# Kernel optimization log

Hardware: AMD Instinct MI355X
Metric: run time of the kernel (lower is better)

## Reference

```python
import jax, jax.numpy as jnp
import numpy as np

B, LQ, D, NH, NL, NP, DFFN = 16, 900, 256, 8, 4, 4, 2048
HD = D // NH
SHAPES = [(128, 128), (64, 64), (32, 32), (16, 16)]
LIN = sum(h * w for h, w in SHAPES)


def setup_inputs():
    ks = jax.random.split(jax.random.key(0), 24)
    p = lambda k, s: jax.random.normal(k, s, jnp.float32) * 0.02
    z = lambda s: jnp.zeros(s, jnp.float32)
    return {
        "queries": jax.random.normal(ks[0], (B, LQ, D), jnp.float32),
        "features": jax.random.normal(ks[1], (B, LIN, D), jnp.float32),
        "reference_points": jax.random.uniform(ks[2], (B, LQ, NL, 2), jnp.float32),
        "q_pos": jax.random.normal(ks[3], (B, LQ, D), jnp.float32),
        "in_proj_w": p(ks[4], (3 * D, D)), "in_proj_b": z((3 * D,)),
        "out_proj_w": p(ks[5], (D, D)), "out_proj_b": z((D,)),
        "value_proj_w": p(ks[6], (D, D)), "value_proj_b": z((D,)),
        "samp_w": p(ks[7], (NH * NL * NP * 2, D)),
        "samp_b": jax.random.uniform(ks[8], (NH * NL * NP * 2,), jnp.float32, -0.5, 0.5),
        "attw_w": p(ks[9], (NH * NL * NP, D)), "attw_b": z((NH * NL * NP,)),
        "msout_w": p(ks[10], (D, D)), "msout_b": z((D,)),
        "ffn_w1": p(ks[11], (DFFN, D)), "ffn_b1": z((DFFN,)),
        "ffn_w2": p(ks[12], (D, DFFN)), "ffn_b2": z((D,)),
        "ln1_g": jnp.ones((D,), jnp.float32), "ln1_b": z((D,)),
        "ln2_g": jnp.ones((D,), jnp.float32), "ln2_b": z((D,)),
        "ln3_g": jnp.ones((D,), jnp.float32), "ln3_b": z((D,)),
        "kv_spatial_shapes": np.array(SHAPES, np.int32),
        "level_start_index": np.concatenate([[0], np.cumsum([h * w for h, w in SHAPES])[:-1]]).astype(np.int32),
    }


def _ln(x, g, b, eps=1e-5):
    m = x.mean(-1, keepdims=True)
    v = ((x - m) ** 2).mean(-1, keepdims=True)
    return (x - m) * jax.lax.rsqrt(v + eps) * g + b


def _mha(q, k, v, wqkv, bqkv, wo, bo):
    wq, wk, wv = wqkv[:D], wqkv[D:2 * D], wqkv[2 * D:]
    bq, bk, bv = bqkv[:D], bqkv[D:2 * D], bqkv[2 * D:]
    qh = (q @ wq.T + bq).reshape(B, LQ, NH, HD)
    kh = (k @ wk.T + bk).reshape(B, LQ, NH, HD)
    vh = (v @ wv.T + bv).reshape(B, LQ, NH, HD)
    s = jnp.einsum("bqhd,bkhd->bhqk", qh, kh) / jnp.sqrt(jnp.float32(HD))
    a = jax.nn.softmax(s, axis=-1)
    o = jnp.einsum("bhqk,bkhd->bqhd", a, vh).reshape(B, LQ, D)
    return o @ wo.T + bo


def _ms_deform(value, loc, attw):
    # value (B,LIN,NH,HD); loc (B,LQ,NH,NL,NP,2) normalized; attw (B,LQ,NH,NL,NP)
    out = jnp.zeros((B, LQ, NH, HD), jnp.float32)
    start = 0
    for l, (hl, wl) in enumerate(SHAPES):
        v = value[:, start:start + hl * wl].transpose(0, 2, 1, 3)  # (B,NH,hl*wl,HD)
        g = loc[:, :, :, l]  # (B,LQ,NH,NP,2)
        # grid_sample align_corners=False pixel coords
        x = g[..., 0] * wl - 0.5
        y = g[..., 1] * hl - 0.5
        x0 = jnp.floor(x); y0 = jnp.floor(y)
        fx = x - x0; fy = y - y0
        x0 = x0.astype(jnp.int32); y0 = y0.astype(jnp.int32)
        acc = jnp.zeros((B, LQ, NH, NP, HD), jnp.float32)
        for dy, wy in ((0, 1.0 - fy), (1, fy)):
            for dx, wx in ((0, 1.0 - fx), (1, fx)):
                xi = x0 + dx; yi = y0 + dy
                valid = (xi >= 0) & (xi < wl) & (yi >= 0) & (yi < hl)
                idx = jnp.clip(yi, 0, hl - 1) * wl + jnp.clip(xi, 0, wl - 1)
                idx = idx.transpose(0, 2, 1, 3).reshape(B, NH, LQ * NP)
                s = jnp.take_along_axis(v, idx[..., None], axis=2)
                s = s.reshape(B, NH, LQ, NP, HD).transpose(0, 2, 1, 3, 4)
                w = jnp.where(valid, wy * wx, 0.0)  # zero-padding outside
                acc = acc + s * w[..., None]
        out = out + (acc * attw[:, :, :, l, :, None]).sum(3)
        start += hl * wl
    return out.reshape(B, LQ, D)


def reference(queries, features, reference_points, q_pos, in_proj_w, in_proj_b, out_proj_w, out_proj_b, value_proj_w, value_proj_b, samp_w, samp_b, attw_w, attw_b, msout_w, msout_b, ffn_w1, ffn_b1, ffn_w2, ffn_b2, ln1_g, ln1_b, ln2_g, ln2_b, ln3_g, ln3_b, kv_spatial_shapes, level_start_index):
    qk = queries + q_pos
    x = _ln(queries + _mha(qk, qk, queries, in_proj_w, in_proj_b, out_proj_w, out_proj_b), ln1_g, ln1_b)
    # deformable multi-scale cross attention
    q2 = x + q_pos
    value = (features @ value_proj_w.T + value_proj_b).reshape(B, LIN, NH, HD)
    off = (q2 @ samp_w.T + samp_b).reshape(B, LQ, NH, NL, NP, 2)
    attw = jax.nn.softmax((q2 @ attw_w.T + attw_b).reshape(B, LQ, NH, NL * NP), axis=-1).reshape(B, LQ, NH, NL, NP)
    norm = jnp.stack([jnp.asarray(kv_spatial_shapes)[:, 1], jnp.asarray(kv_spatial_shapes)[:, 0]], -1).astype(jnp.float32)  # (NL,2)=(W,H)
    loc = reference_points[:, :, None, :, None, :] + off / norm[None, None, None, :, None, :]
    ms = _ms_deform(value, loc, attw) @ msout_w.T + msout_b
    x = _ln(x + ms, ln2_g, ln2_b)
    ffn = jax.nn.relu(x @ ffn_w1.T + ffn_b1) @ ffn_w2.T + ffn_b2
    return _ln(x + ffn, ln3_g, ln3_b)
```

## Files before the change

kernel.cpp:

```cpp
#include <hip/hip_runtime.h>
#include <hip/hip_bf16.h>
#include <math.h>

#define B_    16
#define LQ_   900
#define D_    256
#define NH_   8
#define HD_   32
#define NL_   4
#define NP_   4
#define DFFN_ 2048
#define LIN_  21760

typedef unsigned short u16;
typedef __attribute__((ext_vector_type(8))) short bf16x8;
typedef __attribute__((ext_vector_type(4))) float f32x4;

__device__ __forceinline__ short f2bf(float f) {
    unsigned u = __float_as_uint(f);
    u += 0x7fffu + ((u >> 16) & 1u);
    return (short)(u >> 16);
}
__device__ __forceinline__ float bf2f(u16 u) {
    return __uint_as_float(((unsigned)u) << 16);
}

#define WOFF_INPROJ  0
#define WOFF_OUTPROJ 196608
#define WOFF_VALPROJ 262144
#define WOFF_SAMP    327680
#define WOFF_ATTW    393216
#define WOFF_MSOUT   425984
#define WOFF_FFN1    491520
#define WOFF_FFN2    1015808
#define WTOTAL       1540096

__global__ __launch_bounds__(256) void wprep_kernel(const float* __restrict__ s0,
                                                    const float* __restrict__ s1,
                                                    const float* __restrict__ s2,
                                                    const float* __restrict__ s3,
                                                    const float* __restrict__ s4,
                                                    const float* __restrict__ s5,
                                                    const float* __restrict__ s6,
                                                    const float* __restrict__ s7,
                                                    u16* __restrict__ Wb) {
    int i8 = (blockIdx.x * 256 + threadIdx.x) * 8;
    if (i8 >= WTOTAL) return;
    const float* src; int rel;
    if      (i8 < WOFF_OUTPROJ) { src = s0; rel = i8; }
    else if (i8 < WOFF_VALPROJ) { src = s1; rel = i8 - WOFF_OUTPROJ; }
    else if (i8 < WOFF_SAMP)    { src = s2; rel = i8 - WOFF_VALPROJ; }
    else if (i8 < WOFF_ATTW)    { src = s3; rel = i8 - WOFF_SAMP; }
    else if (i8 < WOFF_MSOUT)   { src = s4; rel = i8 - WOFF_ATTW; }
    else if (i8 < WOFF_FFN1)    { src = s5; rel = i8 - WOFF_MSOUT; }
    else if (i8 < WOFF_FFN2)    { src = s6; rel = i8 - WOFF_FFN1; }
    else                        { src = s7; rel = i8 - WOFF_FFN2; }
    float4 v0 = *(const float4*)(src + rel);
    float4 v1 = *(const float4*)(src + rel + 4);
    short o[8];
    o[0] = f2bf(v0.x); o[1] = f2bf(v0.y); o[2] = f2bf(v0.z); o[3] = f2bf(v0.w);
    o[4] = f2bf(v1.x); o[5] = f2bf(v1.y); o[6] = f2bf(v1.z); o[7] = f2bf(v1.w);
    *(bf16x8*)(Wb + i8) = *(bf16x8*)o;
}

__global__ __launch_bounds__(256) void add_bf16_kernel(const float* __restrict__ a,
                                                       const float* __restrict__ b,
                                                       u16* __restrict__ osum,
                                                       u16* __restrict__ oa,
                                                       size_t n4) {
    size_t i = (size_t)blockIdx.x * blockDim.x + threadIdx.x;
    if (i >= n4) return;
    float4 x = ((const float4*)a)[i];
    float4 y = ((const float4*)b)[i];
    ushort4 s;
    s.x = (u16)f2bf(x.x + y.x); s.y = (u16)f2bf(x.y + y.y);
    s.z = (u16)f2bf(x.z + y.z); s.w = (u16)f2bf(x.w + y.w);
    ((ushort4*)osum)[i] = s;
    if (oa) {
        ushort4 q;
        q.x = (u16)f2bf(x.x); q.y = (u16)f2bf(x.y);
        q.z = (u16)f2bf(x.z); q.w = (u16)f2bf(x.w);
        ((ushort4*)oa)[i] = q;
    }
}

#define LDK 40
template <typename TA, typename TC>
__global__ __launch_bounds__(256) void gemm2_kernel(const TA* __restrict__ A,
                                                    const u16* __restrict__ W,
                                                    const float* __restrict__ bias,
                                                    const float* __restrict__ res,
                                                    TC* __restrict__ C,
                                                    int M, int N, int K, int relu) {
    __shared__ __align__(16) u16 As[2][128 * LDK];
    __shared__ __align__(16) u16 Bs[2][128 * LDK];

    const int n0 = blockIdx.x * 128;
    const int m0 = blockIdx.y * 128;
    const int t  = threadIdx.x;

    const int srow = t >> 1;
    const int scol = (t & 1) << 4;

    const int lane = t & 63;
    const int lr   = lane & 15;
    const int kg   = lane >> 4;
    const int wid  = t >> 6;
    const int wr   = wid >> 1;
    const int wc   = wid & 1;

    f32x4 acc[4][4] = {};

    const int  nk  = K >> 5;
    const int  gm  = m0 + srow;
    const bool mok = (gm < M);

    const float* af32 = (const float*)A + (size_t)(mok ? gm : 0) * K + scol;
    const u16*   ab16 = (const u16*)A + (size_t)(mok ? gm : 0) * K + scol;
    const u16*   wp   = W + (size_t)(n0 + srow) * K + scol;

    float4 af[4];
    bf16x8 ab[2];
    bf16x8 wf[2];

    if constexpr (sizeof(TA) == 4) {
        if (mok) {
            #pragma unroll
            for (int q = 0; q < 4; ++q) af[q] = *(const float4*)(af32 + q * 4);
        } else {
            #pragma unroll
            for (int q = 0; q < 4; ++q) af[q] = make_float4(0.f, 0.f, 0.f, 0.f);
        }
    } else {
        if (mok) { ab[0] = *(const bf16x8*)ab16; ab[1] = *(const bf16x8*)(ab16 + 8); }
        else {
            #pragma unroll
            for (int q = 0; q < 8; ++q) { ab[0][q] = 0; ab[1][q] = 0; }
        }
    }
    wf[0] = *(const bf16x8*)wp;
    wf[1] = *(const bf16x8*)(wp + 8);

    for (int kt = 0; kt < nk; ++kt) {
        const int cur = kt & 1;
        if constexpr (sizeof(TA) == 4) {
            short tmp[16];
            #pragma unroll
            for (int q = 0; q < 4; ++q) {
                tmp[q * 4 + 0] = f2bf(af[q].x);
                tmp[q * 4 + 1] = f2bf(af[q].y);
                tmp[q * 4 + 2] = f2bf(af[q].z);
                tmp[q * 4 + 3] = f2bf(af[q].w);
            }
            *(bf16x8*)&As[cur][srow * LDK + scol]     = *(bf16x8*)tmp;
            *(bf16x8*)&As[cur][srow * LDK + scol + 8] = *(bf16x8*)(tmp + 8);
        } else {
            *(bf16x8*)&As[cur][srow * LDK + scol]     = ab[0];
            *(bf16x8*)&As[cur][srow * LDK + scol + 8] = ab[1];
        }
        *(bf16x8*)&Bs[cur][srow * LDK + scol]     = wf[0];
        *(bf16x8*)&Bs[cur][srow * LDK + scol + 8] = wf[1];

        if (kt + 1 < nk) {
            const int k1 = (kt + 1) << 5;
            if constexpr (sizeof(TA) == 4) {
                if (mok) {
                    #pragma unroll
                    for (int q = 0; q < 4; ++q) af[q] = *(const float4*)(af32 + k1 + q * 4);
                }
            } else {
                if (mok) {
                    ab[0] = *(const bf16x8*)(ab16 + k1);
                    ab[1] = *(const bf16x8*)(ab16 + k1 + 8);
                }
            }
            wf[0] = *(const bf16x8*)(wp + k1);
            wf[1] = *(const bf16x8*)(wp + k1 + 8);
        }

        __syncthreads();

        const u16* pA = &As[cur][(wr * 64 + lr) * LDK + kg * 8];
        const u16* pB = &Bs[cur][(wc * 64 + lr) * LDK + kg * 8];
        bf16x8 a[4], b[4];
        #pragma unroll
        for (int i = 0; i < 4; ++i) a[i] = *(const bf16x8*)(pA + i * 16 * LDK);
        #pragma unroll
        for (int j = 0; j < 4; ++j) b[j] = *(const bf16x8*)(pB + j * 16 * LDK);
        #pragma unroll
        for (int i = 0; i < 4; ++i)
            #pragma unroll
            for (int j = 0; j < 4; ++j)
                acc[i][j] = __builtin_amdgcn_mfma_f32_16x16x32_bf16(a[i], b[j], acc[i][j], 0, 0, 0);
    }

    #pragma unroll
    for (int i = 0; i < 4; ++i) {
        #pragma unroll
        for (int j = 0; j < 4; ++j) {
            const int n = n0 + wc * 64 + j * 16 + lr;
            const float bn = bias[n];
            #pragma unroll
            for (int r = 0; r < 4; ++r) {
                const int m = m0 + wr * 64 + i * 16 + kg * 4 + r;
                if (m < M) {
                    float v = acc[i][j][r] + bn;
                    if (res)  v += res[(size_t)m * N + n];
                    if (relu) v = fmaxf(v, 0.f);
                    if constexpr (sizeof(TC) == 4) C[(size_t)m * N + n] = v;
                    else                           C[(size_t)m * N + n] = (TC)(u16)f2bf(v);
                }
            }
        }
    }
}

#define LDA2 40
#define LDP  72
__global__ __launch_bounds__(256) void attn_mfma_kernel(const u16* __restrict__ Qg,
                                                        const u16* __restrict__ Kg,
                                                        const u16* __restrict__ Vg,
                                                        u16* __restrict__ Og) {
    __shared__ __align__(16) u16 Ks[64 * LDA2];
    __shared__ __align__(16) u16 Vs[64 * LDA2];
    __shared__ __align__(16) u16 Ps[4][16 * LDP];

    const int qt = blockIdx.x, h = blockIdx.y, b = blockIdx.z;
    const int t  = threadIdx.x;
    const int wq = t >> 6;
    const int lane = t & 63;
    const int l15  = lane & 15;
    const int g    = lane >> 4;
    const int q0   = qt * 64;

    const int srow = t >> 2;
    const int sd   = (t & 3) * 8;

    int qrow = q0 + wq * 16 + l15;
    if (qrow > LQ_ - 1) qrow = LQ_ - 1;
    const bf16x8 qfrag = *(const bf16x8*)(Qg + ((size_t)(b * LQ_) + qrow) * D_ + h * HD_ + g * 8);

    float m_i = -1e30f, l_i = 0.f;
    f32x4 o_acc[2] = {};
    const float scale = 0.17677669529663687f;

    for (int k0 = 0; k0 < 960; k0 += 64) {
        {
            int kr = k0 + srow;
            bf16x8 kv, vv;
            if (kr < LQ_) {
                kv = *(const bf16x8*)(Kg + ((size_t)(b * LQ_) + kr) * D_ + h * HD_ + sd);
                vv = *(const bf16x8*)(Vg + ((size_t)(b * LQ_) + kr) * D_ + h * HD_ + sd);
            } else {
                #pragma unroll
                for (int j = 0; j < 8; ++j) { kv[j] = 0; vv[j] = 0; }
            }
            *(bf16x8*)&Ks[srow * LDA2 + sd] = kv;
            *(bf16x8*)&Vs[srow * LDA2 + sd] = vv;
        }
        __syncthreads();

        float p[4][4];
        float tmax = -1e30f;
        #pragma unroll
        for (int kt = 0; kt < 4; ++kt) {
            bf16x8 af = *(const bf16x8*)&Ks[(kt * 16 + l15) * LDA2 + g * 8];
            f32x4 c = {0.f, 0.f, 0.f, 0.f};
            c = __builtin_amdgcn_mfma_f32_16x16x32_bf16(af, qfrag, c, 0, 0, 0);
            #pragma unroll
            for (int r = 0; r < 4; ++r) {
                int kglob = k0 + kt * 16 + g * 4 + r;
                float s = (kglob < LQ_) ? c[r] * scale : -1e30f;
                p[kt][r] = s;
                tmax = fmaxf(tmax, s);
            }
        }
        tmax = fmaxf(tmax, __shfl_xor(tmax, 16));
        tmax = fmaxf(tmax, __shfl_xor(tmax, 32));
        float newm = fmaxf(m_i, tmax);
        float corr = __expf(m_i - newm);
        float rs = 0.f;
        #pragma unroll
        for (int kt = 0; kt < 4; ++kt) {
            #pragma unroll
            for (int r = 0; r < 4; ++r) {
                float e = __expf(p[kt][r] - newm);
                p[kt][r] = e;
                rs += e;
            }
            ushort4 pk;
            pk.x = (u16)f2bf(p[kt][0]);
            pk.y = (u16)f2bf(p[kt][1]);
            pk.z = (u16)f2bf(p[kt][2]);
            pk.w = (u16)f2bf(p[kt][3]);
            *(ushort4*)&Ps[wq][l15 * LDP + kt * 16 + g * 4] = pk;
        }
        rs += __shfl_xor(rs, 16);
        rs += __shfl_xor(rs, 32);
        l_i = l_i * corr + rs;
        m_i = newm;

        #pragma unroll
        for (int r = 0; r < 4; ++r) {
            float cq = __shfl(corr, g * 4 + r);
// ... 14 lines not shown
            }
        }
        __syncthreads();
    }

    float il = 1.f / l_i;
    #pragma unroll
    for (int r = 0; r < 4; ++r) {
        float ilq = __shfl(il, g * 4 + r);
        int q = q0 + wq * 16 + g * 4 + r;
        if (q < LQ_) {
            u16* dst = Og + ((size_t)(b * LQ_) + q) * D_ + h * HD_ + l15;
            dst[0]  = (u16)f2bf(o_acc[0][r] * ilq);
            dst[16] = (u16)f2bf(o_acc[1][r] * ilq);
        }
    }
}

__global__ __launch_bounds__(256) void ln_kernel(const float* __restrict__ X,
                                                 const float* __restrict__ g,
                                                 const float* __restrict__ bb,
                                                 float* __restrict__ Y,
                                                 u16* __restrict__ Yb, int M) {
    int row  = blockIdx.x * 4 + (threadIdx.x >> 6);
    int lane = threadIdx.x & 63;
    if (row >= M) return;
    const float* x = X + (size_t)row * D_;
    float4 v = *(const float4*)(x + lane * 4);
    float s = v.x + v.y + v.z + v.w;
    #pragma unroll
    for (int o = 32; o >= 1; o >>= 1) s += __shfl_xor(s, o);
    float mean = s * (1.f / D_);
    float dx0 = v.x - mean, dx1 = v.y - mean, dx2 = v.z - mean, dx3 = v.w - mean;
    float ss = dx0 * dx0 + dx1 * dx1 + dx2 * dx2 + dx3 * dx3;
    #pragma unroll
    for (int o = 32; o >= 1; o >>= 1) ss += __shfl_xor(ss, o);
    float rstd = rsqrtf(ss * (1.f / D_) + 1e-5f);
    float4 gv = *(const float4*)(g + lane * 4);
    float4 bv = *(const float4*)(bb + lane * 4);
    float4 out;
    out.x = dx0 * rstd * gv.x + bv.x;
    out.y = dx1 * rstd * gv.y + bv.y;
    out.z = dx2 * rstd * gv.z + bv.z;
    out.w = dx3 * rstd * gv.w + bv.w;
    *(float4*)(Y + (size_t)row * D_ + lane * 4) = out;
    if (Yb) {
        ushort4 ob;
        ob.x = (u16)f2bf(out.x); ob.y = (u16)f2bf(out.y);
        ob.z = (u16)f2bf(out.z); ob.w = (u16)f2bf(out.w);
        *(ushort4*)(Yb + (size_t)row * D_ + lane * 4) = ob;
    }
}

__global__ __launch_bounds__(256) void softmax16_kernel(const float* __restrict__ X,
                                                        float* __restrict__ Y,
                                                        int rows) {
    int r = blockIdx.x * blockDim.x + threadIdx.x;
    if (r >= rows) return;
    const float* x = X + (size_t)r * 16;
    float m = -1e30f;
    #pragma unroll
    for (int i = 0; i < 16; ++i) m = fmaxf(m, x[i]);
    float e[16], s = 0.f;
    #pragma unroll
    for (int i = 0; i < 16; ++i) { e[i] = expf(x[i] - m); s += e[i]; }
    float inv = 1.f / s;
    float* y = Y + (size_t)r * 16;
    #pragma unroll
    for (int i = 0; i < 16; ++i) y[i] = e[i] * inv;
}

__global__ __launch_bounds__(256) void msdeform2_kernel(const u16* __restrict__ value,
                                                        const float* __restrict__ ref,
                                                        const float* __restrict__ off,
                                                        const float* __restrict__ attw,
                                                        u16* __restrict__ out) {
    const int levH[4] = {128, 64, 32, 16};
    const int levW[4] = {128, 64, 32, 16};
    const int levS[4] = {0, 16384, 20480, 21504};

    int gid = blockIdx.x * 256 + threadIdx.x;
    int d8  = gid & 3;
    int bqh = gid >> 2;
    int h   = bqh & (NH_ - 1);
    int bq  = bqh >> 3;
    int b   = bq / LQ_;

    const float* refp = ref  + (size_t)bq * NL_ * 2;
    const float* offp = off  + (size_t)bq * 256 + h * 32;
    const float* awp  = attw + (size_t)bq * 128 + h * 16;
    const u16* vbase  = value + (size_t)b * LIN_ * D_ + h * HD_ + d8 * 8;

    float acc[8] = {};
    #pragma unroll
    for (int l = 0; l < NL_; ++l) {
        float rx = refp[l * 2 + 0], ry = refp[l * 2 + 1];
        const int wl = levW[l], hl = levH[l];
        const u16* vlev = vbase + (size_t)levS[l] * D_;
        #pragma unroll
        for (int p = 0; p < NP_; ++p) {
            float ox = offp[(l * NP_ + p) * 2 + 0];
            float oy = offp[(l * NP_ + p) * 2 + 1];
            float x = rx * wl + ox - 0.5f;
            float y = ry * hl + oy - 0.5f;
            float x0f = floorf(x), y0f = floorf(y);
            float fx = x - x0f, fy = y - y0f;
            int x0 = (int)x0f, y0 = (int)y0f;
            float aw = awp[l * NP_ + p];
            #pragma unroll
            for (int dy = 0; dy < 2; ++dy) {
                int   yi = y0 + dy;
                float wy = dy ? fy : 1.f - fy;
                bool  vy = (yi >= 0) && (yi < hl);
                int   yc = min(max(yi, 0), hl - 1);
                #pragma unroll
                for (int dx = 0; dx < 2; ++dx) {
                    int   xi = x0 + dx;
                    float wx = dx ? fx : 1.f - fx;
                    bool  vx = (xi >= 0) && (xi < wl);
                    int   xc = min(max(xi, 0), wl - 1);
                    float w  = (vx && vy) ? aw * wy * wx : 0.f;
                    bf16x8 v = *(const bf16x8*)(vlev + (size_t)(yc * wl + xc) * D_);
                    #pragma unroll
                    for (int j = 0; j < 8; ++j)
                        acc[j] += w * bf2f((u16)v[j]);
                }
            }
        }
    }
    short o[8];
    #pragma unroll
    for (int j = 0; j < 8; ++j) o[j] = f2bf(acc[j]);
    *(bf16x8*)(out + (size_t)bq * D_ + h * HD_ + d8 * 8) = *(bf16x8*)o;
}

extern "C" void kernel_launch(void* const* d_in, const int* in_sizes, int n_in,
                              void* d_out, int out_size, void* d_ws, size_t ws_size,
                              hipStream_t stream) {
    const float* queries      = (const float*)d_in[0];
    const float* features     = (const float*)d_in[1];
    const float* refpts       = (const float*)d_in[2];
    const float* q_pos        = (const float*)d_in[3];
    const float* in_proj_w    = (const float*)d_in[4];
    const float* in_proj_b    = (const float*)d_in[5];
    const float* out_proj_w   = (const float*)d_in[6];
    const float* out_proj_b   = (const float*)d_in[7];
    const float* value_proj_w = (const float*)d_in[8];
    const float* value_proj_b = (const float*)d_in[9];
    const float* samp_w       = (const float*)d_in[10];
    const float* samp_b       = (const float*)d_in[11];
    const float* attw_w       = (const float*)d_in[12];
    const float* attw_b       = (const float*)d_in[13];
    const float* msout_w      = (const float*)d_in[14];
    const float* msout_b      = (const float*)d_in[15];
    const float* ffn_w1       = (const float*)d_in[16];
    const float* ffn_b1       = (const float*)d_in[17];
    const float* ffn_w2       = (const float*)d_in[18];
    const float* ffn_b2       = (const float*)d_in[19];
    const float* ln1_g        = (const float*)d_in[20];
    const float* ln1_b        = (const float*)d_in[21];
    const float* ln2_g        = (const float*)d_in[22];
    const float* ln2_b        = (const float*)d_in[23];
    const float* ln3_g        = (const float*)d_in[24];
    const float* ln3_b        = (const float*)d_in[25];

    float* ws = (float*)d_ws;
    const size_t NQ = (size_t)B_ * LQ_ * D_;
    float* bufB = ws;
    float* bufC = ws + NQ;
    float* bufF = ws + 2 * NQ;
    float* bufD = ws + 3 * NQ;
    u16* U    = (u16*)(ws + 4 * NQ);
    u16* qkb  = U;
    u16* qb   = U + NQ;
    u16* q2b  = U + 2 * NQ;
    u16* Qb   = U + 3 * NQ;
    u16* Kb   = U + 4 * NQ;
    u16* Vb   = U + 5 * NQ;
    u16* Ob   = U + 6 * NQ;
    u16* MSb  = U + 7 * NQ;
    u16* LN2b = U + 8 * NQ;
    u16* VALb = U + 9 * NQ;
    u16* H1b  = VALb + (size_t)B_ * LIN_ * D_;
    u16* Wb   = H1b + (size_t)B_ * LQ_ * DFFN_;

    const int M  = B_ * LQ_;
    const int MV = B_ * LIN_;
    const int GY = (M + 127) / 128;

    wprep_kernel<<<752, 256, 0, stream>>>(in_proj_w, out_proj_w, value_proj_w, samp_w,
                                          attw_w, msout_w, ffn_w1, ffn_w2, Wb);

    add_bf16_kernel<<<3600, 256, 0, stream>>>(queries, q_pos, qkb, qb, NQ / 4);

    gemm2_kernel<u16, u16><<<dim3(2, GY), 256, 0, stream>>>(qkb, Wb + WOFF_INPROJ,          in_proj_b,       nullptr, Qb, M, 256, 256, 0);
    gemm2_kernel<u16, u16><<<dim3(2, GY), 256, 0, stream>>>(qkb, Wb + WOFF_INPROJ + 65536,  in_proj_b + 256, nullptr, Kb, M, 256, 256, 0);
    gemm2_kernel<u16, u16><<<dim3(2, GY), 256, 0, stream>>>(qb,  Wb + WOFF_INPROJ + 131072, in_proj_b + 512, nullptr, Vb, M, 256, 256, 0);

    attn_mfma_kernel<<<dim3(15, NH_, B_), 256, 0, stream>>>(Qb, Kb, Vb, Ob);

    gemm2_kernel<u16, float><<<dim3(2, GY), 256, 0, stream>>>(Ob, Wb + WOFF_OUTPROJ, out_proj_b, queries, bufB, M, 256, 256, 0);
    ln_kernel<<<3600, 256, 0, stream>>>(bufB, ln1_g, ln1_b, bufF, nullptr, M);

    add_bf16_kernel<<<3600, 256, 0, stream>>>(bufF, q_pos, q2b, nullptr, NQ / 4);

    gemm2_kernel<float, u16><<<dim3(2, MV / 128), 256, 0, stream>>>(features, Wb + WOFF_VALPROJ, value_proj_b, nullptr, VALb, MV, 256, 256, 0);

    gemm2_kernel<u16, float><<<dim3(2, GY), 256, 0, stream>>>(q2b, Wb + WOFF_SAMP, samp_b, nullptr, bufB, M, 256, 256, 0);
    gemm2_kernel<u16, float><<<dim3(1, GY), 256, 0, stream>>>(q2b, Wb + WOFF_ATTW, attw_b, nullptr, bufC, M, 128, 256, 0);

    softmax16_kernel<<<450, 256, 0, stream>>>(bufC, bufD, B_ * LQ_ * NH_);

    msdeform2_kernel<<<1800, 256, 0, stream>>>(VALb, refpts, bufB, bufD, MSb);

    gemm2_kernel<u16, float><<<dim3(2, GY), 256, 0, stream>>>(MSb, Wb + WOFF_MSOUT, msout_b, bufF, bufB, M, 256, 256, 0);
    ln_kernel<<<3600, 256, 0, stream>>>(bufB, ln2_g, ln2_b, bufC, LN2b, M);

    gemm2_kernel<u16, u16><<<dim3(16, GY), 256, 0, stream>>>(LN2b, Wb + WOFF_FFN1, ffn_b1, nullptr, H1b, M, 2048, 256, 1);

    gemm2_kernel<u16, float><<<dim3(2, GY), 256, 0, stream>>>(H1b, Wb + WOFF_FFN2, ffn_b2, bufC, bufB, M, 256, 2048, 0);
    ln_kernel<<<3600, 256, 0, stream>>>(bufB, ln3_g, ln3_b, (float*)d_out, nullptr, M);
}
```

Measured before the change: 1.055 ms.

## Add weight-stationary register GEMM for K=256 layers and fuse Q/K and samp/attw projections

Introduces a wavefront-level weight-stationary GEMM that keeps a 32-column slice of the weight in registers and streams 16-row A tiles with double-buffered loads, skipping LDS and block barriers. It replaces the LDS-tiled GEMM for every K=256 projection. The Q and K projections are merged into one N=512 output, and the sampling-offset and attention-weight projections into one N=384 output, with the attention, softmax and deformable-sampling kernels reindexed to match. A packed bias buffer is prepared, and the workspace is resized for the wider fused output. The trade-off is higher register pressure and more A reloads across column slices in exchange for fewer launches and no LDS staging.

```diff
diff --git a/kernel.cpp b/kernel.cpp
--- a/kernel.cpp
+++ b/kernel.cpp
@@ -63,6 +63,38 @@
     *(bf16x8*)(Wb + i8) = *(bf16x8*)o;
 }
 
+#define BOFF_INPROJ  0
+#define BOFF_OUTPROJ 768
+#define BOFF_VALPROJ 1024
+#define BOFF_SAMPATT 1280
+#define BOFF_MSOUT   1664
+#define BOFF_FFN1    1920
+#define BOFF_FFN2    3968
+#define BTOTAL       4224
+
+__global__ __launch_bounds__(256) void bprep_kernel(const float* __restrict__ b0,
+                                                    const float* __restrict__ b1,
+                                                    const float* __restrict__ b2,
+                                                    const float* __restrict__ b3,
+                                                    const float* __restrict__ b4,
+                                                    const float* __restrict__ b5,
+                                                    const float* __restrict__ b6,
+                                                    const float* __restrict__ b7,
+                                                    float* __restrict__ Bb) {
+    int i = blockIdx.x * 256 + threadIdx.x;
+    if (i >= BTOTAL) return;
+    const float* s; int rel;
+    if      (i < BOFF_OUTPROJ) { s = b0; rel = i; }
+    else if (i < BOFF_VALPROJ) { s = b1; rel = i - BOFF_OUTPROJ; }
+    else if (i < BOFF_SAMPATT) { s = b2; rel = i - BOFF_VALPROJ; }
+    else if (i < 1536)         { s = b3; rel = i - BOFF_SAMPATT; }
+    else if (i < BOFF_MSOUT)   { s = b4; rel = i - 1536; }
+    else if (i < BOFF_FFN1)    { s = b5; rel = i - BOFF_MSOUT; }
+    else if (i < BOFF_FFN2)    { s = b6; rel = i - BOFF_FFN1; }
+    else                       { s = b7; rel = i - BOFF_FFN2; }
+    Bb[i] = s[rel];
+}
+
 __global__ __launch_bounds__(256) void add_bf16_kernel(const float* __restrict__ a,
                                                        const float* __restrict__ b,
                                                        u16* __restrict__ osum,
@@ -84,6 +116,113 @@
     }
 }
 
+template <typename TA, typename TC>
+__global__ __launch_bounds__(256) void wsgemm_kernel(const TA* __restrict__ A,
+                                                     const u16* __restrict__ W,
+                                                     const float* __restrict__ bias,
+                                                     const float* __restrict__ res,
+                                                     TC* __restrict__ C,
+                                                     int MT, int NS, int CH, int N, int relu) {
+    const int lane = threadIdx.x & 63;
+    const int l15  = lane & 15;
+    const int g    = lane >> 4;
+    const int wid  = blockIdx.x * 4 + (threadIdx.x >> 6);
+    const int nchunks = (MT + CH - 1) / CH;
+    if (wid >= NS * nchunks) return;
+    const int ns = wid % NS;
+    const int n0 = ns * 32;
+    int mt = (wid / NS) * CH;
+    const int mtend = (mt + CH < MT) ? mt + CH : MT;
+
+    bf16x8 w0[8], w1[8];
+    {
+        const u16* wp0 = W + (size_t)(n0 + l15) * 256 + g * 8;
+        const u16* wp1 = W + (size_t)(n0 + 16 + l15) * 256 + g * 8;
+        #pragma unroll
+        for (int ks = 0; ks < 8; ++ks) {
+            w0[ks] = *(const bf16x8*)(wp0 + ks * 32);
+            w1[ks] = *(const bf16x8*)(wp1 + ks * 32);
+        }
+    }
+    const float bn0 = bias[n0 + l15];
+    const float bn1 = bias[n0 + 16 + l15];
+
+    auto compute_store = [&](const bf16x8 (&a)[8], int m0) {
+        f32x4 acc0 = {0.f, 0.f, 0.f, 0.f}, acc1 = {0.f, 0.f, 0.f, 0.f};
+        #pragma unroll
+        for (int ks = 0; ks < 8; ++ks) {
+            acc0 = __builtin_amdgcn_mfma_f32_16x16x32_bf16(a[ks], w0[ks], acc0, 0, 0, 0);
+            acc1 = __builtin_amdgcn_mfma_f32_16x16x32_bf16(a[ks], w1[ks], acc1, 0, 0, 0);
+        }
+        #pragma unroll
+        for (int r = 0; r < 4; ++r) {
+            const int m = m0 + g * 4 + r;
+            float v0 = acc0[r] + bn0;
+            float v1 = acc1[r] + bn1;
+            if (res) {
+                v0 += res[(size_t)m * N + n0 + l15];
+                v1 += res[(size_t)m * N + n0 + 16 + l15];
+            }
+            if (relu) { v0 = fmaxf(v0, 0.f); v1 = fmaxf(v1, 0.f); }
+            if constexpr (sizeof(TC) == 4) {
+                C[(size_t)m * N + n0 + l15]      = v0;
+                C[(size_t)m * N + n0 + 16 + l15] = v1;
+            } else {
+                C[(size_t)m * N + n0 + l15]      = (TC)(u16)f2bf(v0);
+                C[(size_t)m * N + n0 + 16 + l15] = (TC)(u16)f2bf(v1);
+            }
+        }
+    };
+
+    if constexpr (sizeof(TA) == 2) {
+        const u16* Ab = (const u16*)A;
+        bf16x8 p[8], q[8];
+        {
+            const u16* ar = Ab + (size_t)(mt * 16 + l15) * 256 + g * 8;
+            #pragma unroll
+            for (int ks = 0; ks < 8; ++ks) p[ks] = *(const bf16x8*)(ar + ks * 32);
+        }
+        while (true) {
+            if (mt + 1 < mtend) {
+                const u16* ar = Ab + (size_t)((mt + 1) * 16 + l15) * 256 + g * 8;
+                #pragma unroll
+                for (int ks = 0; ks < 8; ++ks) q[ks] = *(const bf16x8*)(ar + ks * 32);
+            }
+            compute_store(p, mt * 16);
+            if (++mt >= mtend) break;
+            if (mt + 1 < mtend) {
+                const u16* ar = Ab + (size_t)((mt + 1) * 16 + l15) * 256 + g * 8;
+                #pragma unroll
+                for (int ks = 0; ks < 8; ++ks) p[ks] = *(const bf16x8*)(ar + ks * 32);
+            }
+            compute_store(q, mt * 16);
+            if (++mt >= mtend) break;
+        }
+    } else {
+        const float* Af = (const float*)A;
+        for (; mt < mtend; ++mt) {
+            const float* ar = Af + (size_t)(mt * 16 + l15) * 256 + g * 8;
+            float4 f0[8], f1[8];
+            #pragma unroll
+            for (int ks = 0; ks < 8; ++ks) {
+                f0[ks] = *(const float4*)(ar + ks * 32);
+                f1[ks] = *(const float4*)(ar + ks * 32 + 4);
+            }
+            bf16x8 a[8];
+            #pragma unroll
+            for (int ks = 0; ks < 8; ++ks) {
+                short tmp[8];
+                tmp[0] = f2bf(f0[ks].x); tmp[1] = f2bf(f0[ks].y);
+                tmp[2] = f2bf(f0[ks].z); tmp[3] = f2bf(f0[ks].w);
+                tmp[4] = f2bf(f1[ks].x); tmp[5] = f2bf(f1[ks].y);
+                tmp[6] = f2bf(f1[ks].z); tmp[7] = f2bf(f1[ks].w);
+                a[ks] = *(bf16x8*)tmp;
+            }
+            compute_store(a, mt * 16);
+        }
+    }
+}
+
 #define LDK 40
 template <typename TA, typename TC>
 __global__ __launch_bounds__(256) void gemm2_kernel(const TA* __restrict__ A,
@@ -115,64 +254,30 @@
     const int  gm  = m0 + srow;
     const bool mok = (gm < M);
 
-    const float* af32 = (const float*)A + (size_t)(mok ? gm : 0) * K + scol;
-    const u16*   ab16 = (const u16*)A + (size_t)(mok ? gm : 0) * K + scol;
-    const u16*   wp   = W + (size_t)(n0 + srow) * K + scol;
-
-    float4 af[4];
-    bf16x8 ab[2];
-    bf16x8 wf[2];
-
-    if constexpr (sizeof(TA) == 4) {
-        if (mok) {
-            #pragma unroll
-            for (int q = 0; q < 4; ++q) af[q] = *(const float4*)(af32 + q * 4);
-        } else {
-            #pragma unroll
-            for (int q = 0; q < 4; ++q) af[q] = make_float4(0.f, 0.f, 0.f, 0.f);
-        }
-    } else {
-        if (mok) { ab[0] = *(const bf16x8*)ab16; ab[1] = *(const bf16x8*)(ab16 + 8); }
-        else {
-            #pragma unroll
-            for (int q = 0; q < 8; ++q) { ab[0][q] = 0; ab[1][q] = 0; }
-        }
+    const u16* ab16 = (const u16*)A + (size_t)(mok ? gm : 0) * K + scol;
+    const u16* wp   = W + (size_t)(n0 + srow) * K + scol;
+
+    bf16x8 ab[2], wf[2];
+    if (mok) { ab[0] = *(const bf16x8*)ab16; ab[1] = *(const bf16x8*)(ab16 + 8); }
+    else {
+        #pragma unroll
+        for (int q = 0; q < 8; ++q) { ab[0][q] = 0; ab[1][q] = 0; }
     }
     wf[0] = *(const bf16x8*)wp;
     wf[1] = *(const bf16x8*)(wp + 8);
 
     for (int kt = 0; kt < nk; ++kt) {
         const int cur = kt & 1;
-        if constexpr (sizeof(TA) == 4) {
-            short tmp[16];
-            #pragma unroll
-            for (int q = 0; q < 4; ++q) {
-                tmp[q * 4 + 0] = f2bf(af[q].x);
-                tmp[q * 4 + 1] = f2bf(af[q].y);
-                tmp[q * 4 + 2] = f2bf(af[q].z);
-                tmp[q * 4 + 3] = f2bf(af[q].w);
-            }
-            *(bf16x8*)&As[cur][srow * LDK + scol]     = *(bf16x8*)tmp;
-            *(bf16x8*)&As[cur][srow * LDK + scol + 8] = *(bf16x8*)(tmp + 8);
-        } else {
-            *(bf16x8*)&As[cur][srow * LDK + scol]     = ab[0];
-            *(bf16x8*)&As[cur][srow * LDK + scol + 8] = ab[1];
-        }
+        *(bf16x8*)&As[cur][srow * LDK + scol]     = ab[0];
+        *(bf16x8*)&As[cur][srow * LDK + scol + 8] = ab[1];
         *(bf16x8*)&Bs[cur][srow * LDK + scol]     = wf[0];
         *(bf16x8*)&Bs[cur][srow * LDK + scol + 8] = wf[1];
 
         if (kt + 1 < nk) {
             const int k1 = (kt + 1) << 5;
-            if constexpr (sizeof(TA) == 4) {
-                if (mok) {
-                    #pragma unroll
-                    for (int q = 0; q < 4; ++q) af[q] = *(const float4*)(af32 + k1 + q * 4);
-                }
-            } else {
-                if (mok) {
-                    ab[0] = *(const bf16x8*)(ab16 + k1);
-                    ab[1] = *(const bf16x8*)(ab16 + k1 + 8);
-                }
+            if (mok) {
+                ab[0] = *(const bf16x8*)(ab16 + k1);
+                ab[1] = *(const bf16x8*)(ab16 + k1 + 8);
             }
             wf[0] = *(const bf16x8*)(wp + k1);
             wf[1] = *(const bf16x8*)(wp + k1 + 8);
@@ -217,8 +322,7 @@
 
 #define LDA2 40
 #define LDP  72
-__global__ __launch_bounds__(256) void attn_mfma_kernel(const u16* __restrict__ Qg,
-                                                        const u16* __restrict__ Kg,
+__global__ __launch_bounds__(256) void attn_mfma_kernel(const u16* __restrict__ QKg,
                                                         const u16* __restrict__ Vg,
                                                         u16* __restrict__ Og) {
     __shared__ __align__(16) u16 Ks[64 * LDA2];
@@ -238,7 +342,7 @@
 
     int qrow = q0 + wq * 16 + l15;
     if (qrow > LQ_ - 1) qrow = LQ_ - 1;
-    const bf16x8 qfrag = *(const bf16x8*)(Qg + ((size_t)(b * LQ_) + qrow) * D_ + h * HD_ + g * 8);
+    const bf16x8 qfrag = *(const bf16x8*)(QKg + ((size_t)(b * LQ_) + qrow) * 512 + h * HD_ + g * 8);
 
     float m_i = -1e30f, l_i = 0.f;
     f32x4 o_acc[2] = {};
@@ -249,7 +353,7 @@
             int kr = k0 + srow;
             bf16x8 kv, vv;
             if (kr < LQ_) {
-                kv = *(const bf16x8*)(Kg + ((size_t)(b * LQ_) + kr) * D_ + h * HD_ + sd);
+                kv = *(const bf16x8*)(QKg + ((size_t)(b * LQ_) + kr) * 512 + 256 + h * HD_ + sd);
                 vv = *(const bf16x8*)(Vg + ((size_t)(b * LQ_) + kr) * D_ + h * HD_ + sd);
             } else {
                 #pragma unroll
@@ -370,12 +474,12 @@
     }
 }
 
-__global__ __launch_bounds__(256) void softmax16_kernel(const float* __restrict__ X,
-                                                        float* __restrict__ Y,
-                                                        int rows) {
+__global__ __launch_bounds__(256) void softmax16v_kernel(const float* __restrict__ X,
+                                                         float* __restrict__ Y,
+                                                         int rows) {
     int r = blockIdx.x * blockDim.x + threadIdx.x;
     if (r >= rows) return;
-    const float* x = X + (size_t)r * 16;
+    const float* x = X + (size_t)(r >> 3) * 384 + 256 + (r & 7) * 16;
     float m = -1e30f;
     #pragma unroll
     for (int i = 0; i < 16; ++i) m = fmaxf(m, x[i]);
@@ -405,7 +509,7 @@
     int b   = bq / LQ_;
 
     const float* refp = ref  + (size_t)bq * NL_ * 2;
-    const float* offp = off  + (size_t)bq * 256 + h * 32;
+    const float* offp = off  + (size_t)bq * 384 + h * 32;
     const float* awp  = attw + (size_t)bq * 128 + h * 16;
     const u16* vbase  = value + (size_t)b * LIN_ * D_ + h * HD_ + d8 * 8;
 
@@ -485,15 +589,14 @@
     float* ws = (float*)d_ws;
     const size_t NQ = (size_t)B_ * LQ_ * D_;
     float* bufB = ws;
-    float* bufC = ws + NQ;
-    float* bufF = ws + 2 * NQ;
-    float* bufD = ws + 3 * NQ;
-    u16* U    = (u16*)(ws + 4 * NQ);
+    float* bufC = ws + 3 * NQ / 2;
+    float* bufF = bufC + NQ;
+    float* bufD = bufF + NQ;
+    u16* U    = (u16*)(bufD + NQ);
     u16* qkb  = U;
     u16* qb   = U + NQ;
     u16* q2b  = U + 2 * NQ;
-    u16* Qb   = U + 3 * NQ;
-    u16* Kb   = U + 4 * NQ;
+    u16* QKb  = U + 3 * NQ;
     u16* Vb   = U + 5 * NQ;
     u16* Ob   = U + 6 * NQ;
     u16* MSb  = U + 7 * NQ;
@@ -501,41 +604,40 @@
     u16* VALb = U + 9 * NQ;
     u16* H1b  = VALb + (size_t)B_ * LIN_ * D_;
     u16* Wb   = H1b + (size_t)B_ * LQ_ * DFFN_;
-
-    const int M  = B_ * LQ_;
-    const int MV = B_ * LIN_;
-    const int GY = (M + 127) / 128;
+    float* Bb = (float*)(Wb + WTOTAL);
+
+    const int M = B_ * LQ_;
 
     wprep_kernel<<<752, 256, 0, stream>>>(in_proj_w, out_proj_w, value_proj_w, samp_w,
                                           attw_w, msout_w, ffn_w1, ffn_w2, Wb);
+    bprep_kernel<<<17, 256, 0, stream>>>(in_proj_b, out_proj_b, value_proj_b, samp_b,
+                                         attw_b, msout_b, ffn_b1, ffn_b2, Bb);
 
     add_bf16_kernel<<<3600, 256, 0, stream>>>(queries, q_pos, qkb, qb, NQ / 4);
 
-    gemm2_kernel<u16, u16><<<dim3(2, GY), 256, 0, stream>>>(qkb, Wb + WOFF_INPROJ,          in_proj_b,       nullptr, Qb, M, 256, 256, 0);
-    gemm2_kernel<u16, u16><<<dim3(2, GY), 256, 0, stream>>>(qkb, Wb + WOFF_INPROJ + 65536,  in_proj_b + 256, nullptr, Kb, M, 256, 256, 0);
-    gemm2_kernel<u16, u16><<<dim3(2, GY), 256, 0, stream>>>(qb,  Wb + WOFF_INPROJ + 131072, in_proj_b + 512, nullptr, Vb, M, 256, 256, 0);
-
-    attn_mfma_kernel<<<dim3(15, NH_, B_), 256, 0, stream>>>(Qb, Kb, Vb, Ob);
-
-    gemm2_kernel<u16, float><<<dim3(2, GY), 256, 0, stream>>>(Ob, Wb + WOFF_OUTPROJ, out_proj_b, queries, bufB, M, 256, 256, 0);
-    ln_kernel<<<3600, 256, 0, stream>>>(bufB, ln1_g, ln1_b, bufF, nullptr, M);
+    wsgemm_kernel<u16, u16><<<900, 256, 0, stream>>>(qkb, Wb + WOFF_INPROJ, Bb + BOFF_INPROJ, nullptr, QKb, 900, 16, 4, 512, 0);
+    wsgemm_kernel<u16, u16><<<450, 256, 0, stream>>>(qb, Wb + WOFF_INPROJ + 131072, Bb + BOFF_INPROJ + 512, nullptr, Vb, 900, 8, 4, 256, 0);
+
+    attn_mfma_kernel<<<dim3(15, NH_, B_), 256, 0, stream>>>(QKb, Vb, Ob);
+
+    wsgemm_kernel<u16, float><<<450, 256, 0, stream>>>(Ob, Wb + WOFF_OUTPROJ, Bb + BOFF_OUTPROJ, queries, bufC, 900, 8, 4, 256, 0);
+    ln_kernel<<<3600, 256, 0, stream>>>(bufC, ln1_g, ln1_b, bufF, nullptr, M);
 
     add_bf16_kernel<<<3600, 256, 0, stream>>>(bufF, q_pos, q2b, nullptr, NQ / 4);
 
-    gemm2_kernel<float, u16><<<dim3(2, MV / 128), 256, 0, stream>>>(features, Wb + WOFF_VALPROJ, value_proj_b, nullptr, VALb, MV, 256, 256, 0);
-
-    gemm2_kernel<u16, float><<<dim3(2, GY), 256, 0, stream>>>(q2b, Wb + WOFF_SAMP, samp_b, nullptr, bufB, M, 256, 256, 0);
-    gemm2_kernel<u16, float><<<dim3(1, GY), 256, 0, stream>>>(q2b, Wb + WOFF_ATTW, attw_b, nullptr, bufC, M, 128, 256, 0);
-
-    softmax16_kernel<<<450, 256, 0, stream>>>(bufC, bufD, B_ * LQ_ * NH_);
+    wsgemm_kernel<float, u16><<<1360, 256, 0, stream>>>(features, Wb + WOFF_VALPROJ, Bb + BOFF_VALPROJ, nullptr, VALb, 21760, 8, 32, 256, 0);
+
+    wsgemm_kernel<u16, float><<<675, 256, 0, stream>>>(q2b, Wb + WOFF_SAMP, Bb + BOFF_SAMPATT, nullptr, bufB, 900, 12, 4, 384, 0);
+
+    softmax16v_kernel<<<450, 256, 0, stream>>>(bufB, bufD, B_ * LQ_ * NH_);
 
     msdeform2_kernel<<<1800, 256, 0, stream>>>(VALb, refpts, bufB, bufD, MSb);
 
-    gemm2_kernel<u16, float><<<dim3(2, GY), 256, 0, stream>>>(MSb, Wb + WOFF_MSOUT, msout_b, bufF, bufB, M, 256, 256, 0);
-    ln_kernel<<<3600, 256, 0, stream>>>(bufB, ln2_g, ln2_b, bufC, LN2b, M);
-
-    gemm2_kernel<u16, u16><<<dim3(16, GY), 256, 0, stream>>>(LN2b, Wb + WOFF_FFN1, ffn_b1, nullptr, H1b, M, 2048, 256, 1);
-
-    gemm2_kernel<u16, float><<<dim3(2, GY), 256, 0, stream>>>(H1b, Wb + WOFF_FFN2, ffn_b2, bufC, bufB, M, 256, 2048, 0);
-    ln_kernel<<<3600, 256, 0, stream>>>(bufB, ln3_g, ln3_b, (float*)d_out, nullptr, M);
-}
+    wsgemm_kernel<u16, float><<<450, 256, 0, stream>>>(MSb, Wb + WOFF_MSOUT, Bb + BOFF_MSOUT, bufF, bufC, 900, 8, 4, 256, 0);
+    ln_kernel<<<3600, 256, 0, stream>>>(bufC, ln2_g, ln2_b, bufD, LN2b, M);
+
+    wsgemm_kernel<u16, u16><<<3600, 256, 0, stream>>>(LN2b, Wb + WOFF_FFN1, Bb + BOFF_FFN1, nullptr, H1b, 900, 64, 4, 2048, 1);
+
+    gemm2_kernel<u16, float><<<dim3(2, 113), 256, 0, stream>>>(H1b, Wb + WOFF_FFN2, ffn_b2, bufD, bufC, M, 256, 2048, 0);
+    ln_kernel<<<3600, 256, 0, stream>>>(bufC, ln3_g, ln3_b, (float*)d_out, nullptr, M);
+}
```

After: 1.402 ms. 32.9% more time.

## Merge Q/K and sampling/attention projections, deepen GEMM global prefetch

Applied to the files above, without the earlier changes.

Q and K projections become a single N=512 GEMM writing an interleaved QK buffer, which the attention kernel now reads with stride 512. The sampling-offset and attention-weight projections become a single N=384 GEMM, and the softmax and deformable kernels index into that combined layout. The GEMM kernel now keeps two register stages of global loads in flight ahead of the LDS write. Biases are packed into a contiguous buffer so the concatenated projections see contiguous biases. The intent is fewer launches, one fewer read of the shared input, and better hiding of global-load latency, at the cost of more registers in the GEMM.

```diff
diff --git a/kernel.cpp b/kernel.cpp
--- a/kernel.cpp
+++ b/kernel.cpp
@@ -63,6 +63,38 @@
     *(bf16x8*)(Wb + i8) = *(bf16x8*)o;
 }
 
+#define BOFF_INPROJ  0
+#define BOFF_OUTPROJ 768
+#define BOFF_VALPROJ 1024
+#define BOFF_SAMPATT 1280
+#define BOFF_MSOUT   1664
+#define BOFF_FFN1    1920
+#define BOFF_FFN2    3968
+#define BTOTAL       4224
+
+__global__ __launch_bounds__(256) void bprep_kernel(const float* __restrict__ b0,
+                                                    const float* __restrict__ b1,
+                                                    const float* __restrict__ b2,
+                                                    const float* __restrict__ b3,
+                                                    const float* __restrict__ b4,
+                                                    const float* __restrict__ b5,
+                                                    const float* __restrict__ b6,
+                                                    const float* __restrict__ b7,
+                                                    float* __restrict__ Bb) {
+    int i = blockIdx.x * 256 + threadIdx.x;
+    if (i >= BTOTAL) return;
+    const float* s; int rel;
+    if      (i < BOFF_OUTPROJ) { s = b0; rel = i; }
+    else if (i < BOFF_VALPROJ) { s = b1; rel = i - BOFF_OUTPROJ; }
+    else if (i < BOFF_SAMPATT) { s = b2; rel = i - BOFF_VALPROJ; }
+    else if (i < 1536)         { s = b3; rel = i - BOFF_SAMPATT; }
+    else if (i < BOFF_MSOUT)   { s = b4; rel = i - 1536; }
+    else if (i < BOFF_FFN1)    { s = b5; rel = i - BOFF_MSOUT; }
+    else if (i < BOFF_FFN2)    { s = b6; rel = i - BOFF_FFN1; }
+    else                       { s = b7; rel = i - BOFF_FFN2; }
+    Bb[i] = s[rel];
+}
+
 __global__ __launch_bounds__(256) void add_bf16_kernel(const float* __restrict__ a,
                                                        const float* __restrict__ b,
                                                        u16* __restrict__ osum,
@@ -86,7 +118,7 @@
 
 #define LDK 40
 template <typename TA, typename TC>
-__global__ __launch_bounds__(256) void gemm2_kernel(const TA* __restrict__ A,
+__global__ __launch_bounds__(256) void gemm3_kernel(const TA* __restrict__ A,
                                                     const u16* __restrict__ W,
                                                     const float* __restrict__ bias,
                                                     const float* __restrict__ res,
@@ -98,10 +130,8 @@
     const int n0 = blockIdx.x * 128;
     const int m0 = blockIdx.y * 128;
     const int t  = threadIdx.x;
-
     const int srow = t >> 1;
     const int scol = (t & 1) << 4;
-
     const int lane = t & 63;
     const int lr   = lane & 15;
     const int kg   = lane >> 4;
@@ -119,69 +149,42 @@
     const u16*   ab16 = (const u16*)A + (size_t)(mok ? gm : 0) * K + scol;
     const u16*   wp   = W + (size_t)(n0 + srow) * K + scol;
 
-    float4 af[4];
-    bf16x8 ab[2];
-    bf16x8 wf[2];
-
-    if constexpr (sizeof(TA) == 4) {
-        if (mok) {
-            #pragma unroll
-            for (int q = 0; q < 4; ++q) af[q] = *(const float4*)(af32 + q * 4);
-        } else {
-            #pragma unroll
-            for (int q = 0; q < 4; ++q) af[q] = make_float4(0.f, 0.f, 0.f, 0.f);
-        }
-    } else {
-        if (mok) { ab[0] = *(const bf16x8*)ab16; ab[1] = *(const bf16x8*)(ab16 + 8); }
-        else {
-            #pragma unroll
-            for (int q = 0; q < 8; ++q) { ab[0][q] = 0; ab[1][q] = 0; }
-        }
-    }
-    wf[0] = *(const bf16x8*)wp;
-    wf[1] = *(const bf16x8*)(wp + 8);
-
-    for (int kt = 0; kt < nk; ++kt) {
-        const int cur = kt & 1;
-        if constexpr (sizeof(TA) == 4) {
-            short tmp[16];
-            #pragma unroll
-            for (int q = 0; q < 4; ++q) {
-                tmp[q * 4 + 0] = f2bf(af[q].x);
-                tmp[q * 4 + 1] = f2bf(af[q].y);
-                tmp[q * 4 + 2] = f2bf(af[q].z);
-                tmp[q * 4 + 3] = f2bf(af[q].w);
-            }
-            *(bf16x8*)&As[cur][srow * LDK + scol]     = *(bf16x8*)tmp;
-            *(bf16x8*)&As[cur][srow * LDK + scol + 8] = *(bf16x8*)(tmp + 8);
-        } else {
-            *(bf16x8*)&As[cur][srow * LDK + scol]     = ab[0];
-            *(bf16x8*)&As[cur][srow * LDK + scol + 8] = ab[1];
-        }
-        *(bf16x8*)&Bs[cur][srow * LDK + scol]     = wf[0];
-        *(bf16x8*)&Bs[cur][srow * LDK + scol + 8] = wf[1];
-
-        if (kt + 1 < nk) {
-            const int k1 = (kt + 1) << 5;
-            if constexpr (sizeof(TA) == 4) {
-                if (mok) {
-                    #pragma unroll
-                    for (int q = 0; q < 4; ++q) af[q] = *(const float4*)(af32 + k1 + q * 4);
-                }
-            } else {
-                if (mok) {
-                    ab[0] = *(const bf16x8*)(ab16 + k1);
-                    ab[1] = *(const bf16x8*)(ab16 + k1 + 8);
-                }
-            }
-            wf[0] = *(const bf16x8*)(wp + k1);
-            wf[1] = *(const bf16x8*)(wp + k1 + 8);
-        }
-
-        __syncthreads();
-
-        const u16* pA = &As[cur][(wr * 64 + lr) * LDK + kg * 8];
-        const u16* pB = &Bs[cur][(wc * 64 + lr) * LDK + kg * 8];
+    float4 af0[4], af1[4];
+    bf16x8 ab0[2], ab1[2];
+    bf16x8 wf0[2], wf1[2];
+    if (!mok) {
+        #pragma unroll
+        for (int q = 0; q < 4; ++q) af0[q] = af1[q] = make_float4(0.f, 0.f, 0.f, 0.f);
+        #pragma unroll
+        for (int q = 0; q < 8; ++q) { ab0[0][q] = 0; ab0[1][q] = 0; ab1[0][q] = 0; ab1[1][q] = 0; }
+    }
+
+#define GLOAD_A_F(afX, kt_) do { if (mok) { \
+        _Pragma("unroll") for (int q = 0; q < 4; ++q) afX[q] = *(const float4*)(af32 + ((kt_) << 5) + q * 4); } } while (0)
+#define GLOAD_A_B(abX, kt_) do { if (mok) { \
+        abX[0] = *(const bf16x8*)(ab16 + ((kt_) << 5)); \
+        abX[1] = *(const bf16x8*)(ab16 + ((kt_) << 5) + 8); } } while (0)
+#define GLOAD_W(wfX, kt_) do { \
+        wfX[0] = *(const bf16x8*)(wp + ((kt_) << 5)); \
+        wfX[1] = *(const bf16x8*)(wp + ((kt_) << 5) + 8); } while (0)
+
+#define DSWRITE(bufI, afX, abX, wfX) do { \
+        if constexpr (sizeof(TA) == 4) { \
+            short tmp[16]; \
+            _Pragma("unroll") for (int q = 0; q < 4; ++q) { \
+                tmp[q * 4 + 0] = f2bf(afX[q].x); tmp[q * 4 + 1] = f2bf(afX[q].y); \
+                tmp[q * 4 + 2] = f2bf(afX[q].z); tmp[q * 4 + 3] = f2bf(afX[q].w); } \
+            *(bf16x8*)&As[bufI][srow * LDK + scol]     = *(bf16x8*)tmp; \
+            *(bf16x8*)&As[bufI][srow * LDK + scol + 8] = *(bf16x8*)(tmp + 8); \
+        } else { \
+            *(bf16x8*)&As[bufI][srow * LDK + scol]     = abX[0]; \
+            *(bf16x8*)&As[bufI][srow * LDK + scol + 8] = abX[1]; } \
+        *(bf16x8*)&Bs[bufI][srow * LDK + scol]     = wfX[0]; \
+        *(bf16x8*)&Bs[bufI][srow * LDK + scol + 8] = wfX[1]; } while (0)
+
+    auto domfma = [&](const u16* bufA, const u16* bufB) {
+        const u16* pA = bufA + (wr * 64 + lr) * LDK + kg * 8;
+        const u16* pB = bufB + (wc * 64 + lr) * LDK + kg * 8;
         bf16x8 a[4], b[4];
         #pragma unroll
         for (int i = 0; i < 4; ++i) a[i] = *(const bf16x8*)(pA + i * 16 * LDK);
@@ -192,7 +195,35 @@
             #pragma unroll
             for (int j = 0; j < 4; ++j)
                 acc[i][j] = __builtin_amdgcn_mfma_f32_16x16x32_bf16(a[i], b[j], acc[i][j], 0, 0, 0);
-    }
+    };
+
+    if constexpr (sizeof(TA) == 4) { GLOAD_A_F(af0, 0); GLOAD_A_F(af1, 1); }
+    else                           { GLOAD_A_B(ab0, 0); GLOAD_A_B(ab1, 1); }
+    GLOAD_W(wf0, 0); GLOAD_W(wf1, 1);
+
+    int kt = 0;
+    while (true) {
+        DSWRITE(0, af0, ab0, wf0);
+        if (kt + 2 < nk) {
+            if constexpr (sizeof(TA) == 4) GLOAD_A_F(af0, kt + 2); else GLOAD_A_B(ab0, kt + 2);
+            GLOAD_W(wf0, kt + 2);
+        }
+        __syncthreads();
+        domfma(&As[0][0], &Bs[0][0]);
+        if (++kt >= nk) break;
+        DSWRITE(1, af1, ab1, wf1);
+        if (kt + 2 < nk) {
+            if constexpr (sizeof(TA) == 4) GLOAD_A_F(af1, kt + 2); else GLOAD_A_B(ab1, kt + 2);
+            GLOAD_W(wf1, kt + 2);
+        }
+        __syncthreads();
+        domfma(&As[1][0], &Bs[1][0]);
+        if (++kt >= nk) break;
+    }
+#undef GLOAD_A_F
+#undef GLOAD_A_B
+#undef GLOAD_W
+#undef DSWRITE
 
     #pragma unroll
     for (int i = 0; i < 4; ++i) {
@@ -217,8 +248,7 @@
 
 #define LDA2 40
 #define LDP  72
-__global__ __launch_bounds__(256) void attn_mfma_kernel(const u16* __restrict__ Qg,
-                                                        const u16* __restrict__ Kg,
+__global__ __launch_bounds__(256) void attn_mfma_kernel(const u16* __restrict__ QKg,
                                                         const u16* __restrict__ Vg,
                                                         u16* __restrict__ Og) {
     __shared__ __align__(16) u16 Ks[64 * LDA2];
@@ -238,7 +268,7 @@
 
     int qrow = q0 + wq * 16 + l15;
     if (qrow > LQ_ - 1) qrow = LQ_ - 1;
-    const bf16x8 qfrag = *(const bf16x8*)(Qg + ((size_t)(b * LQ_) + qrow) * D_ + h * HD_ + g * 8);
+    const bf16x8 qfrag = *(const bf16x8*)(QKg + ((size_t)(b * LQ_) + qrow) * 512 + h * HD_ + g * 8);
 
     float m_i = -1e30f, l_i = 0.f;
     f32x4 o_acc[2] = {};
@@ -249,7 +279,7 @@
             int kr = k0 + srow;
             bf16x8 kv, vv;
             if (kr < LQ_) {
-                kv = *(const bf16x8*)(Kg + ((size_t)(b * LQ_) + kr) * D_ + h * HD_ + sd);
+                kv = *(const bf16x8*)(QKg + ((size_t)(b * LQ_) + kr) * 512 + 256 + h * HD_ + sd);
                 vv = *(const bf16x8*)(Vg + ((size_t)(b * LQ_) + kr) * D_ + h * HD_ + sd);
             } else {
                 #pragma unroll
@@ -370,12 +400,12 @@
     }
 }
 
-__global__ __launch_bounds__(256) void softmax16_kernel(const float* __restrict__ X,
-                                                        float* __restrict__ Y,
-                                                        int rows) {
+__global__ __launch_bounds__(256) void softmax16v_kernel(const float* __restrict__ X,
+                                                         float* __restrict__ Y,
+                                                         int rows) {
     int r = blockIdx.x * blockDim.x + threadIdx.x;
     if (r >= rows) return;
-    const float* x = X + (size_t)r * 16;
+    const float* x = X + (size_t)(r >> 3) * 384 + 256 + (r & 7) * 16;
     float m = -1e30f;
     #pragma unroll
     for (int i = 0; i < 16; ++i) m = fmaxf(m, x[i]);
@@ -405,7 +435,7 @@
     int b   = bq / LQ_;
 
     const float* refp = ref  + (size_t)bq * NL_ * 2;
-    const float* offp = off  + (size_t)bq * 256 + h * 32;
+    const float* offp = off  + (size_t)bq * 384 + h * 32;
     const float* awp  = attw + (size_t)bq * 128 + h * 16;
     const u16* vbase  = value + (size_t)b * LIN_ * D_ + h * HD_ + d8 * 8;
 
@@ -485,15 +515,14 @@
     float* ws = (float*)d_ws;
     const size_t NQ = (size_t)B_ * LQ_ * D_;
     float* bufB = ws;
-    float* bufC = ws + NQ;
-    float* bufF = ws + 2 * NQ;
-    float* bufD = ws + 3 * NQ;
-    u16* U    = (u16*)(ws + 4 * NQ);
+    float* bufC = ws + 3 * NQ / 2;
+    float* bufF = bufC + NQ;
+    float* bufD = bufF + NQ;
+    u16* U    = (u16*)(bufD + NQ);
     u16* qkb  = U;
     u16* qb   = U + NQ;
     u16* q2b  = U + 2 * NQ;
-    u16* Qb   = U + 3 * NQ;
-    u16* Kb   = U + 4 * NQ;
+    u16* QKb  = U + 3 * NQ;
     u16* Vb   = U + 5 * NQ;
     u16* Ob   = U + 6 * NQ;
     u16* MSb  = U + 7 * NQ;
@@ -501,41 +530,41 @@
     u16* VALb = U + 9 * NQ;
     u16* H1b  = VALb + (size_t)B_ * LIN_ * D_;
     u16* Wb   = H1b + (size_t)B_ * LQ_ * DFFN_;
-
-    const int M  = B_ * LQ_;
-    const int MV = B_ * LIN_;
-    const int GY = (M + 127) / 128;
+    float* Bb = (float*)(Wb + WTOTAL);
+
+    const int M = B_ * LQ_;
+    const int GY = 113;
 
     wprep_kernel<<<752, 256, 0, stream>>>(in_proj_w, out_proj_w, value_proj_w, samp_w,
                                           attw_w, msout_w, ffn_w1, ffn_w2, Wb);
+    bprep_kernel<<<17, 256, 0, stream>>>(in_proj_b, out_proj_b, value_proj_b, samp_b,
+                                         attw_b, msout_b, ffn_b1, ffn_b2, Bb);
 
     add_bf16_kernel<<<3600, 256, 0, stream>>>(queries, q_pos, qkb, qb, NQ / 4);
 
-    gemm2_kernel<u16, u16><<<dim3(2, GY), 256, 0, stream>>>(qkb, Wb + WOFF_INPROJ,          in_proj_b,       nullptr, Qb, M, 256, 256, 0);
-    gemm2_kernel<u16, u16><<<dim3(2, GY), 256, 0, stream>>>(qkb, Wb + WOFF_INPROJ + 65536,  in_proj_b + 256, nullptr, Kb, M, 256, 256, 0);
-    gemm2_kernel<u16, u16><<<dim3(2, GY), 256, 0, stream>>>(qb,  Wb + WOFF_INPROJ + 131072, in_proj_b + 512, nullptr, Vb, M, 256, 256, 0);
-
-    attn_mfma_kernel<<<dim3(15, NH_, B_), 256, 0, stream>>>(Qb, Kb, Vb, Ob);
-
-    gemm2_kernel<u16, float><<<dim3(2, GY), 256, 0, stream>>>(Ob, Wb + WOFF_OUTPROJ, out_proj_b, queries, bufB, M, 256, 256, 0);
-    ln_kernel<<<3600, 256, 0, stream>>>(bufB, ln1_g, ln1_b, bufF, nullptr, M);
+    gemm3_kernel<u16, u16><<<dim3(4, GY), 256, 0, stream>>>(qkb, Wb + WOFF_INPROJ, Bb + BOFF_INPROJ, nullptr, QKb, M, 512, 256, 0);
+    gemm3_kernel<u16, u16><<<dim3(2, GY), 256, 0, stream>>>(qb, Wb + WOFF_INPROJ + 131072, Bb + BOFF_INPROJ + 512, nullptr, Vb, M, 256, 256, 0);
+
+    attn_mfma_kernel<<<dim3(15, NH_, B_), 256, 0, stream>>>(QKb, Vb, Ob);
+
+    gemm3_kernel<u16, float><<<dim3(2, GY), 256, 0, stream>>>(Ob, Wb + WOFF_OUTPROJ, Bb + BOFF_OUTPROJ, queries, bufC, M, 256, 256, 0);
+    ln_kernel<<<3600, 256, 0, stream>>>(bufC, ln1_g, ln1_b, bufF, nullptr, M);
 
     add_bf16_kernel<<<3600, 256, 0, stream>>>(bufF, q_pos, q2b, nullptr, NQ / 4);
 
-    gemm2_kernel<float, u16><<<dim3(2, MV / 128), 256, 0, stream>>>(features, Wb + WOFF_VALPROJ, value_proj_b, nullptr, VALb, MV, 256, 256, 0);
-
-    gemm2_kernel<u16, float><<<dim3(2, GY), 256, 0, stream>>>(q2b, Wb + WOFF_SAMP, samp_b, nullptr, bufB, M, 256, 256, 0);
-    gemm2_kernel<u16, float><<<dim3(1, GY), 256, 0, stream>>>(q2b, Wb + WOFF_ATTW, attw_b, nullptr, bufC, M, 128, 256, 0);
-
-    softmax16_kernel<<<450, 256, 0, stream>>>(bufC, bufD, B_ * LQ_ * NH_);
+    gemm3_kernel<float, u16><<<dim3(2, 2720), 256, 0, stream>>>(features, Wb + WOFF_VALPROJ, Bb + BOFF_VALPROJ, nullptr, VALb, B_ * LIN_, 256, 256, 0);
+
+    gemm3_kernel<u16, float><<<dim3(3, GY), 256, 0, stream>>>(q2b, Wb + WOFF_SAMP, Bb + BOFF_SAMPATT, nullptr, bufB, M, 384, 256, 0);
+
+    softmax16v_kernel<<<450, 256, 0, stream>>>(bufB, bufD, B_ * LQ_ * NH_);
 
     msdeform2_kernel<<<1800, 256, 0, stream>>>(VALb, refpts, bufB, bufD, MSb);
 
-    gemm2_kernel<u16, float><<<dim3(2, GY), 256, 0, stream>>>(MSb, Wb + WOFF_MSOUT, msout_b, bufF, bufB, M, 256, 256, 0);
-    ln_kernel<<<3600, 256, 0, stream>>>(bufB, ln2_g, ln2_b, bufC, LN2b, M);
-
-    gemm2_kernel<u16, u16><<<dim3(16, GY), 256, 0, stream>>>(LN2b, Wb + WOFF_FFN1, ffn_b1, nullptr, H1b, M, 2048, 256, 1);
-
-    gemm2_kernel<u16, float><<<dim3(2, GY), 256, 0, stream>>>(H1b, Wb + WOFF_FFN2, ffn_b2, bufC, bufB, M, 256, 2048, 0);
-    ln_kernel<<<3600, 256, 0, stream>>>(bufB, ln3_g, ln3_b, (float*)d_out, nullptr, M);
-}
+    gemm3_kernel<u16, float><<<dim3(2, GY), 256, 0, stream>>>(MSb, Wb + WOFF_MSOUT, Bb + BOFF_MSOUT, bufF, bufC, M, 256, 256, 0);
+    ln_kernel<<<3600, 256, 0, stream>>>(bufC, ln2_g, ln2_b, bufD, LN2b, M);
+
+    gemm3_kernel<u16, u16><<<dim3(16, GY), 256, 0, stream>>>(LN2b, Wb + WOFF_FFN1, Bb + BOFF_FFN1, nullptr, H1b, M, 2048, 256, 1);
+
+    gemm3_kernel<u16, float><<<dim3(2, GY), 256, 0, stream>>>(H1b, Wb + WOFF_FFN2, Bb + BOFF_FFN2, bufD, bufC, M, 256, 2048, 0);
+    ln_kernel<<<3600, 256, 0, stream>>>(bufC, ln3_g, ln3_b, (float*)d_out, nullptr, M);
+}
```

Result: slower. 1.095 ms (+3.7%).
